# Kernel tuning notes

Measured on AMD Instinct MI355X. Metric: run time of the kernel, lower is better.

The kernel has to match this reference:

```python
import jax, jax.numpy as jnp
import numpy as np
from jax import lax

DIM = 192
HEADS = 6
WS = 8
SHIFT = 4
RED = max(8, DIM // 8)  # 24
HID = 4 * DIM


def _rel_index(ws):
    coords = np.stack(np.meshgrid(np.arange(ws), np.arange(ws), indexing='ij'))  # [2,ws,ws]
    flat = coords.reshape(2, -1)
    rel = (flat[:, :, None] - flat[:, None, :]).transpose(1, 2, 0)  # [T,T,2]
    rel[:, :, 0] += ws - 1
    rel[:, :, 1] += ws - 1
    rel[:, :, 0] *= 2 * ws - 1
    return rel.sum(-1)  # [T,T]


def _build_mask(h, w, ws, shift):
    img = np.zeros((h, w))
    slices = (slice(0, -ws), slice(-ws, -shift), slice(-shift, None))
    cnt = 0
    for hs in slices:
        for wcs in slices:
            img[hs, wcs] = cnt
            cnt += 1
    mw = img.reshape(h // ws, ws, w // ws, ws).transpose(0, 2, 1, 3).reshape(-1, ws * ws)
    diff = mw[:, None, :] - mw[:, :, None]  # [nW,T,T], diff[w,i,j]=mw[w,j]-mw[w,i]
    return np.where(diff != 0, -100.0, 0.0).astype(np.float32)


def _ln(x, g, b):
    m = x.mean(-1, keepdims=True)
    v = ((x - m) ** 2).mean(-1, keepdims=True)
    return (x - m) / jnp.sqrt(v + 1e-5) * g + b


def _conv(x, k, b, pad):
    y = lax.conv_general_dilated(x, k, (1, 1), [(pad, pad), (pad, pad)],
                                 dimension_numbers=('NCHW', 'OIHW', 'NCHW'))
    return y + b[None, :, None, None]


def setup_inputs() -> dict:
    key = jax.random.key(0)
    ks = jax.random.split(key, 16)
    rn = lambda k, s, sc=0.02: jax.random.normal(k, s, dtype=jnp.float32) * sc
    C = DIM
    return {
        'x': jax.random.normal(ks[0], (4, 256 * 256, C), dtype=jnp.float32),
        'ln1_g': jnp.ones((C,), jnp.float32), 'ln1_b': jnp.zeros((C,), jnp.float32),
        'w_qkv': rn(ks[1], (3 * C, C)), 'b_qkv': jnp.zeros((3 * C,), jnp.float32),
        'rel_table': rn(ks[2], ((2 * WS - 1) ** 2, HEADS)),
        'w_proj': rn(ks[3], (C, C)), 'b_proj': jnp.zeros((C,), jnp.float32),
        'ln2_g': jnp.ones((C,), jnp.float32), 'ln2_b': jnp.zeros((C,), jnp.float32),
        'w_fc1': rn(ks[4], (HID, C)), 'b_fc1': jnp.zeros((HID,), jnp.float32),
        'w_fc2': rn(ks[5], (C, HID)), 'b_fc2': jnp.zeros((C,), jnp.float32),
        'conv1_w': rn(ks[6], (RED, C, 1, 1)), 'conv1_b': jnp.zeros((RED,), jnp.float32),
        'conv2_w': rn(ks[7], (RED, RED, 3, 3)), 'conv2_b': jnp.zeros((RED,), jnp.float32),
        'conv3_w': rn(ks[8], (C, RED, 1, 1)), 'conv3_b': jnp.zeros((C,), jnp.float32),
        'se_w1': rn(ks[9], (RED, C)), 'se_w2': rn(ks[10], (C, RED)),
        'h': 256, 'w': 256,
    }


def reference(x, ln1_g, ln1_b, w_qkv, b_qkv, rel_table, w_proj, b_proj,
              ln2_g, ln2_b, w_fc1, b_fc1, w_fc2, b_fc2,
              conv1_w, conv1_b, conv2_w, conv2_b, conv3_w, conv3_b,
              se_w1, se_w2, h, w):
    B, _, C = x.shape
    ws, T, nh = WS, WS * WS, HEADS
    hd = C // nh
    scale = hd ** -0.5

    nx = _ln(x, ln1_g, ln1_b).reshape(B, h, w, C)
    local = nx.transpose(0, 3, 1, 2)  # NCHW for LCE

    # shifted window attention
    sh = jnp.roll(nx, (-SHIFT, -SHIFT), axis=(1, 2))
    win = sh.reshape(B, h // ws, ws, w // ws, ws, C).transpose(0, 1, 3, 2, 4, 5).reshape(-1, T, C)
    qkv = (win @ w_qkv.T + b_qkv).reshape(-1, T, 3, nh, hd).transpose(2, 0, 3, 1, 4)
    q, k, v = qkv[0] * scale, qkv[1], qkv[2]  # [BW, nh, T, hd]
    attn = jnp.einsum('whid,whjd->whij', q, k)  # [BW, nh, T, T]
    bias = rel_table[_rel_index(ws).reshape(-1)].reshape(T, T, nh).transpose(2, 0, 1)
    attn = attn + bias[None]
    mask = jnp.asarray(_build_mask(h, w, ws, SHIFT))  # [nW, T, T]
    nW = mask.shape[0]
    attn = attn.reshape(B, nW, nh, T, T) + mask[None, :, None]
    attn = jax.nn.softmax(attn, axis=-1).reshape(-1, nh, T, T)
    out = jnp.einsum('whij,whjd->whid', attn, v).transpose(0, 2, 1, 3).reshape(-1, T, C)
    out = out @ w_proj.T + b_proj
    out = out.reshape(B, h // ws, w // ws, ws, ws, C).transpose(0, 1, 3, 2, 4, 5).reshape(B, h, w, C)
    out = jnp.roll(out, (SHIFT, SHIFT), axis=(1, 2))

    x1 = x + out.reshape(B, h * w, C)
    n2 = _ln(x1, ln2_g, ln2_b)
    mlp = jax.nn.gelu(n2 @ w_fc1.T + b_fc1, approximate=False) @ w_fc2.T + b_fc2
    x2 = x1 + mlp

    # LocalContextExtractor (SE-style)
    y = _conv(local, conv1_w, conv1_b, 0)
    y = _conv(y, conv2_w, conv2_b, 1)
    y = _conv(y, conv3_w, conv3_b, 0)
    y = jnp.where(y >= 0, y, 0.2 * y)  # LeakyReLU(0.2)
    pooled = y.mean(axis=(2, 3))  # [B, C]
    wgt = jax.nn.sigmoid(jax.nn.relu(pooled @ se_w1.T) @ se_w2.T)
    y = y * wgt[:, :, None, None]
    lc = y.reshape(B, C, h * w).transpose(0, 2, 1)
    return x2 + lc
```

## Files before the change

### kernel.cpp

```cpp
#include <hip/hip_runtime.h>
#include <hip/hip_bf16.h>

typedef unsigned short u16;
typedef unsigned long long u64;
typedef __attribute__((ext_vector_type(8))) short short8x;
typedef __attribute__((ext_vector_type(4))) float f32x4;
typedef __bf16 bf16x8 __attribute__((ext_vector_type(8)));

#define SCALE 0.17677669529663687f

__device__ __forceinline__ u16 f2bf(float f) {
  unsigned u = __builtin_bit_cast(unsigned, f);
  unsigned r = (u + 0x7FFFu + ((u >> 16) & 1u)) >> 16;
  return (u16)r;
}
__device__ __forceinline__ float bf2f(u16 h) {
  return __builtin_bit_cast(float, ((unsigned)h) << 16);
}
__device__ __forceinline__ float gelu_f(float v) {
  float t = v * v;
  float a = __builtin_fmaf(t, -0.07135481627f, -1.59576912161f);
  float e = __expf(v * a);
  return v * __builtin_amdgcn_rcpf(1.0f + e);
}
__device__ __forceinline__ int swz(int row, int col, int ld) {
  return row * ld + ((((col >> 3) ^ (row & 7)) << 3) | (col & 7));
}
__device__ __forceinline__ short8x ldfrag(const u16* s, int row, int kb, int ld) {
  return *(const short8x*)(s + row * ld + (((kb >> 3) ^ (row & 7)) << 3));
}
__device__ __forceinline__ short8x ldg8(const u16* p) { return *(const short8x*)p; }

__device__ __forceinline__ f32x4 MFMA(short8x a, short8x b, f32x4 c) {
  return __builtin_amdgcn_mfma_f32_16x16x32_bf16(
      __builtin_bit_cast(bf16x8, a), __builtin_bit_cast(bf16x8, b), c, 0, 0, 0);
}
__device__ __forceinline__ u64 pack4(float a, float b, float c, float d) {
  return (u64)f2bf(a) | ((u64)f2bf(b) << 16) | ((u64)f2bf(c) << 32) | ((u64)f2bf(d) << 48);
}

__global__ void cvt_kernel(const float* __restrict__ wqkv, const float* __restrict__ wproj,
                           const float* __restrict__ wfc1, const float* __restrict__ wfc2,
                           const float* __restrict__ c1, const float* __restrict__ c3,
                           const float* __restrict__ c2,
                           u16* oq, u16* op, u16* o1, u16* o2, u16* oc1, u16* oc3,
                           float* ow2r) {
  int i = blockIdx.x * 256 + threadIdx.x;
  if (i < 110592) { float f = wqkv[i]; if (i < 36864) f *= SCALE; oq[i] = f2bf(f); return; }
  i -= 110592;
  if (i < 36864) { op[i] = f2bf(wproj[i]); return; }
  i -= 36864;
  if (i < 147456) { o1[i] = f2bf(wfc1[i]); return; }
  i -= 147456;
  if (i < 147456) { o2[i] = f2bf(wfc2[i]); return; }
  i -= 147456;
  if (i < 6144) { int r = i / 192, c = i - r * 192; oc1[i] = (r < 24) ? f2bf(c1[r * 192 + c]) : (u16)0; return; }
  i -= 6144;
  if (i < 6144) { int cc = i >> 5, k = i & 31; oc3[i] = (k < 24) ? f2bf(c3[cc * 24 + k]) : (u16)0; return; }
  i -= 6144;
  if (i < 5184) { int t = i / 576, rr = i - t * 576; int ci = rr / 24, co = rr - ci * 24;
                  ow2r[i] = c2[co * 216 + ci * 9 + t]; }
}

__global__ __launch_bounds__(256) void ln1_kernel(const float* __restrict__ x,
                                                  const float* __restrict__ g,
                                                  const float* __restrict__ b,
                                                  u16* __restrict__ nx) {
  const int wid = threadIdx.x >> 6, lane = threadIdx.x & 63;
  const int row = blockIdx.x * 4 + wid;
  const float* xr = x + row * 192;
  f32x4 v = {0.f, 0.f, 0.f, 0.f};
  if (lane < 48) v = *(const f32x4*)(xr + lane * 4);
  float s = v[0] + v[1] + v[2] + v[3];
  for (int m = 1; m < 64; m <<= 1) s += __shfl_xor(s, m);
  const float mean = s * (1.0f / 192.0f);
  f32x4 d;
#pragma unroll
  for (int r = 0; r < 4; ++r) d[r] = v[r] - mean;
  float q = (lane < 48) ? (d[0] * d[0] + d[1] * d[1] + d[2] * d[2] + d[3] * d[3]) : 0.f;
  for (int m = 1; m < 64; m <<= 1) q += __shfl_xor(q, m);
  const float rstd = rsqrtf(q * (1.0f / 192.0f) + 1e-5f);
  if (lane < 48) {
    const f32x4 gg = *(const f32x4*)(g + lane * 4);
    const f32x4 bb = *(const f32x4*)(b + lane * 4);
    u64 pk = pack4(d[0] * rstd * gg[0] + bb[0], d[1] * rstd * gg[1] + bb[1],
                   d[2] * rstd * gg[2] + bb[2], d[3] * rstd * gg[3] + bb[3]);
    *(u64*)(nx + row * 192 + lane * 4) = pk;
  }
}

__global__ __launch_bounds__(512, 4) void attn_kernel(
    const float* __restrict__ x, const u16* __restrict__ nx,
    const u16* __restrict__ wq, const float* __restrict__ bqkv,
    const float* __restrict__ rel, const u16* __restrict__ wp,
    const float* __restrict__ bproj, u16* __restrict__ vT,
    float* __restrict__ x1out) {
  __shared__ u16 sQK[64 * 384];
  __shared__ float sRel[1350];
  __shared__ int sG[64];

  const int tid = threadIdx.x, blk = blockIdx.x;
  const int b = blk >> 10, wi = (blk >> 5) & 31, wj = blk & 31;
  const int wv = tid >> 6, lane = tid & 63, lr = lane & 15, hi = lane >> 4;
  u16* vTw = vT + blk * 12288;

  for (int i = tid; i < 1350; i += 512) sRel[i] = rel[i];
  if (tid < 64) {
    int si = (wi * 8 + (tid >> 3) + 4) & 255, sj = (wj * 8 + (tid & 7) + 4) & 255;
    sG[tid] = b * 65536 + si * 256 + sj;
  }
  for (int i = tid; i < 64 * 96; i += 512) {
    int r = i / 96, w32 = i - r * 96;
    int si = (wi * 8 + (r >> 3) + 4) & 255, sj = (wj * 8 + (r & 7) + 4) & 255;
    int grow = b * 65536 + si * 256 + sj;
    unsigned v = ((const unsigned*)nx)[grow * 96 + w32];
    ((unsigned*)sQK)[r * 192 + ((((w32 >> 2) ^ (r & 7)) << 2) | (w32 & 3))] = v;
  }
  __syncthreads();

  f32x4 acc[4][4] = {};
  if (wv < 6) {
    const int wbase = wv * 64;
#pragma unroll
    for (int kk = 0; kk < 6; ++kk) {
      short8x Xf[4];
#pragma unroll
      for (int tt = 0; tt < 4; ++tt) Xf[tt] = ldfrag(sQK, tt * 16 + lr, kk * 32 + hi * 8, 384);
#pragma unroll
      for (int wt = 0; wt < 4; ++wt) {
        short8x Wf = ldg8(wq + (wbase + wt * 16 + lr) * 192 + kk * 32 + hi * 8);
#pragma unroll
        for (int tt = 0; tt < 4; ++tt) acc[wt][tt] = MFMA(Wf, Xf[tt], acc[wt][tt]);
      }
    }
  } else {
    const int vbase = (wv - 6) * 96;
#pragma unroll
    for (int half = 0; half < 2; ++half) {
      short8x Bf[3][6];
      float bv[3];
#pragma unroll
      for (int j = 0; j < 3; ++j) {
        const int vc = vbase + (half * 3 + j) * 16 + lr;
#pragma unroll
        for (int kk = 0; kk < 6; ++kk)
          Bf[j][kk] = ldg8(wq + (384 + vc) * 192 + kk * 32 + hi * 8);
        bv[j] = bqkv[384 + vc];
      }
#pragma unroll
      for (int mt = 0; mt < 4; ++mt) {
        f32x4 vacc[3] = {};
#pragma unroll
        for (int kk = 0; kk < 6; ++kk) {
          short8x A = ldfrag(sQK, mt * 16 + lr, kk * 32 + hi * 8, 384);
#pragma unroll
          for (int j = 0; j < 3; ++j) vacc[j] = MFMA(A, Bf[j][kk], vacc[j]);
        }
#pragma unroll
        for (int j = 0; j < 3; ++j) {
          u64 pk = pack4(vacc[j][0] + bv[j], vacc[j][1] + bv[j],
                         vacc[j][2] + bv[j], vacc[j][3] + bv[j]);
          *(u64*)(vTw + (vbase + (half * 3 + j) * 16 + lr) * 64 + mt * 16 + hi * 4) = pk;
        }
      }
    }
  }
  __syncthreads();

  if (wv < 6) {
    const int wbase = wv * 64;
#pragma unroll
    for (int wt = 0; wt < 4; ++wt) {
      const int oc0 = wbase + wt * 16 + hi * 4;
      const f32x4 bq = *(const f32x4*)(bqkv + oc0);
      const float sc = (oc0 < 192) ? SCALE : 1.0f;
#pragma unroll
      for (int tt = 0; tt < 4; ++tt) {
        u64 pk = pack4(acc[wt][tt][0] + bq[0] * sc, acc[wt][tt][1] + bq[1] * sc,
                       acc[wt][tt][2] + bq[2] * sc, acc[wt][tt][3] + bq[3] * sc);
        *(u64*)&sQK[swz(tt * 16 + lr, oc0, 384)] = pk;
      }
    }
  }
  __syncthreads();

  f32x4 S[3][4];
#pragma unroll
  for (int i = 0; i < 3; ++i) {
    const int s = wv + 8 * i, h3 = s >> 2, q = s & 3;
    short8x Aq = ldfrag(sQK, q * 16 + lr, h3 * 32 + hi * 8, 384);
#pragma unroll
    for (int nt = 0; nt < 4; ++nt) {
      short8x Bk = ldfrag(sQK, nt * 16 + lr, 192 + h3 * 32 + hi * 8, 384);
      S[i][nt] = MFMA(Aq, Bk, (f32x4){0.f, 0.f, 0.f, 0.f});
    }
#pragma unroll
    for (int r = 0; r < 4; ++r) {
      const int tI = q * 16 + hi * 4 + r;
      const int tri = tI >> 3, trj = tI & 7;
      const int ui = wi * 8 + tri, vi = wj * 8 + trj;
      const int rgi = (ui >= 248) + (ui >= 252), cgi = (vi >= 248) + (vi >= 252);
#pragma unroll
      for (int nt = 0; nt < 4; ++nt) {
        const int tJ = nt * 16 + lr;
        const int tci = tJ >> 3, tcj = tJ & 7;
        const int idx = (tri - tci + 7) * 15 + (trj - tcj + 7);
        float v = S[i][nt][r] + sRel[idx * 6 + h3];
        const int uj = wi * 8 + tci, vj = wj * 8 + tcj;
        const int rgj = (uj >= 248) + (uj >= 252), cgj = (vj >= 248) + (vj >= 252);
        if ((rgi != rgj) | (cgi != cgj)) v -= 100.0f;
        S[i][nt][r] = v;
      }
    }
#pragma unroll
    for (int r = 0; r < 4; ++r) {
      float mx = fmaxf(fmaxf(S[i][0][r], S[i][1][r]), fmaxf(S[i][2][r], S[i][3][r]));
      mx = fmaxf(mx, __shfl_xor(mx, 1));
      mx = fmaxf(mx, __shfl_xor(mx, 2));
      mx = fmaxf(mx, __shfl_xor(mx, 4));
      mx = fmaxf(mx, __shfl_xor(mx, 8));
      float sm = 0.f;
#pragma unroll
      for (int nt = 0; nt < 4; ++nt) { float e = __expf(S[i][nt][r] - mx); S[i][nt][r] = e; sm += e; }
      sm += __shfl_xor(sm, 1); sm += __shfl_xor(sm, 2);
      sm += __shfl_xor(sm, 4); sm += __shfl_xor(sm, 8);
      const float inv = 1.0f / sm;
#pragma unroll
      for (int nt = 0; nt < 4; ++nt) S[i][nt][r] *= inv;
    }
  }
  __syncthreads();

#pragma unroll
  for (int i = 0; i < 3; ++i) {
    const int s = wv + 8 * i, h3 = s >> 2, q = s & 3;
#pragma unroll
    for (int r = 0; r < 4; ++r)
#pragma unroll
      for (int nt = 0; nt < 4; ++nt)
        sQK[h3 * 4096 + swz(q * 16 + hi * 4 + r, nt * 16 + lr, 64)] = f2bf(S[i][nt][r]);
  }
  __syncthreads();

  f32x4 oacc[3][2] = {};
#pragma unroll
  for (int i = 0; i < 3; ++i) {
    const int t = wv + 8 * i, h3 = t >> 2, dt = (t >> 1) & 1, tth = t & 1;
#pragma unroll
    for (int kk = 0; kk < 2; ++kk) {
      short8x Va = ldg8(vTw + (h3 * 32 + dt * 16 + lr) * 64 + kk * 32 + hi * 8);
#pragma unroll
      for (int t2 = 0; t2 < 2; ++t2) {
        short8x Pf = ldfrag(sQK + h3 * 4096, tth * 32 + t2 * 16 + lr, kk * 32 + hi * 8, 64);
        oacc[i][t2] = MFMA(Va, Pf, oacc[i][t2]);
      }
    }
  }
  __syncthreads();

#pragma unroll
  for (int i = 0; i < 3; ++i) {
    const int t = wv + 8 * i, h3 = t >> 2, dt = (t >> 1) & 1, tth = t & 1;
#pragma unroll
    for (int t2 = 0; t2 < 2; ++t2) {
      u64 pk = pack4(oacc[i][t2][0], oacc[i][t2][1], oacc[i][t2][2], oacc[i][t2][3]);
      *(u64*)&sQK[swz(tth * 32 + t2 * 16 + lr, h3 * 32 + dt * 16 + hi * 4, 192)] = pk;
    }
  }
  __syncthreads();

  {
    const int nw = (wv < 4) ? 2 : 1;
    const int wt0 = (wv < 4) ? wv * 2 : (4 + wv);
    f32x4 pacc[2][4] = {};
#pragma unroll
    for (int kk = 0; kk < 6; ++kk) {
      short8x Of[4];
#pragma unroll
      for (int tt = 0; tt < 4; ++tt) Of[tt] = ldfrag(sQK, tt * 16 + lr, kk * 32 + hi * 8, 192);
      for (int w2 = 0; w2 < nw; ++w2) {
        short8x Wp = ldg8(wp + ((wt0 + w2) * 16 + lr) * 192 + kk * 32 + hi * 8);
#pragma unroll
        for (int tt = 0; tt < 4; ++tt) pacc[w2][tt] = MFMA(Wp, Of[tt], pacc[w2][tt]);
      }
    }
    for (int w2 = 0; w2 < nw; ++w2) {
      const int oc0 = (wt0 + w2) * 16 + hi * 4;
      const f32x4 bb = *(const f32x4*)(bproj + oc0);
#pragma unroll
      for (int tt = 0; tt < 4; ++tt) {
        const int grow = sG[tt * 16 + lr];
        const f32x4 xv = *(const f32x4*)(x + grow * 192 + oc0);
        f32x4 o;
#pragma unroll
        for (int r = 0; r < 4; ++r) o[r] = xv[r] + pacc[w2][tt][r] + bb[r];
        *(f32x4*)(x1out + grow * 192 + oc0) = o;
      }
    }
  }
}

__global__ __launch_bounds__(256) void conv1_kernel(const u16* __restrict__ nx,
                                                    const u16* __restrict__ w1,
                                                    const float* __restrict__ b1,
                                                    float* __restrict__ y1) {
  const int tid = threadIdx.x, wv = tid >> 6, lane = tid & 63, lr = lane & 15, hi = lane >> 4;
  const int g0 = blockIdx.x * 64;
  const int mt = wv;
  short8x Af[6];
#pragma unroll
  for (int kk = 0; kk < 6; ++kk)
    Af[kk] = ldg8(nx + (g0 + mt * 16 + lr) * 192 + kk * 32 + hi * 8);
  const int bI = g0 >> 16;
  const int hw0 = g0 & 65535;
#pragma unroll
  for (int nt = 0; nt < 2; ++nt) {
    f32x4 acc = {0.f, 0.f, 0.f, 0.f};
#pragma unroll
    for (int kk = 0; kk < 6; ++kk) {
      short8x Bf = ldg8(w1 + (nt * 16 + lr) * 192 + kk * 32 + hi * 8);
      acc = MFMA(Af[kk], Bf, acc);
    }
    const int c = nt * 16 + lr;
    if (c < 24) {
      const float bb = b1[c];
#pragma unroll
      for (int r = 0; r < 4; ++r) {
        const int pix = hw0 + mt * 16 + hi * 4 + r;
        y1[(bI * 24 + c) * 65536 + pix] = acc[r] + bb;
      }
    }
  }
}

__global__ __launch_bounds__(256) void conv2_kernel(const float* __restrict__ y1,
                                                    const float* __restrict__ w2r,
                                                    const float* __restrict__ cb2,
                                                    u16* __restrict__ y2) {
  const int j = threadIdx.x;
  const int i = blockIdx.x & 255;
  const int b = blockIdx.x >> 8;
  float acc[24];
#pragma unroll
  for (int r = 0; r < 24; ++r) acc[r] = cb2[r];
  const float* base = y1 + b * 24 * 65536;
  for (int t = 0; t < 9; ++t) {
    const int dh = t / 3 - 1, dw = t % 3 - 1;
    const int ii = i + dh, jj = j + dw;
    const bool ok = (ii >= 0) & (ii < 256) & (jj >= 0) & (jj < 256);
    const int offc = ok ? (ii * 256 + jj) : 0;
    const float* wt = w2r + t * 576;
    float v[24];
#pragma unroll
    for (int ci = 0; ci < 24; ++ci) {
      float vv = base[ci * 65536 + offc];
      v[ci] = ok ? vv : 0.0f;
    }
#pragma unroll
    for (int ci = 0; ci < 24; ++ci)
#pragma unroll
      for (int co = 0; co < 24; ++co)
        acc[co] += v[ci] * wt[ci * 24 + co];
  }
  u16* o = y2 + (b * 65536 + i * 256 + j) * 32;
#pragma unroll
  for (int r = 0; r < 24; ++r) o[r] = f2bf(acc[r]);
  ((unsigned long long*)(o + 24))[0] = 0ull;
  ((unsigned long long*)(o + 24))[1] = 0ull;
}

__global__ __launch_bounds__(256) void conv3_kernel(const u16* __restrict__ y2,
                                                    const u16* __restrict__ w3,
                                                    const float* __restrict__ b3,
                                                    u16* __restrict__ y,
                                                    float* __restrict__ pooled) {
  const int tid = threadIdx.x, wv = tid >> 6, lane = tid & 63, lr = lane & 15, hi = lane >> 4;
  const int g0 = blockIdx.x * 64;
  short8x Af[4];
#pragma unroll
  for (int mt = 0; mt < 4; ++mt)
    Af[mt] = ldg8(y2 + (g0 + mt * 16 + lr) * 32 + hi * 8);
  const int bI = g0 >> 16;
#pragma unroll
  for (int nt0 = 0; nt0 < 3; ++nt0) {
    const int c = (wv * 3 + nt0) * 16 + lr;
    short8x Bf = ldg8(w3 + c * 32 + hi * 8);
    const float bb = b3[c];
    float colsum = 0.f;
#pragma unroll
    for (int mt = 0; mt < 4; ++mt) {
      f32x4 acc = {0.f, 0.f, 0.f, 0.f};
      acc = MFMA(Af[mt], Bf, acc);
#pragma unroll
      for (int r = 0; r < 4; ++r) {
        float v = acc[r] + bb;
        v = (v >= 0.f) ? v : 0.2f * v;
        y[(g0 + mt * 16 + hi * 4 + r) * 192 + c] = f2bf(v);
        colsum += v;
      }
    }
    colsum += __shfl_xor(colsum, 16);
    colsum += __shfl_xor(colsum, 32);
    if (hi == 0) atomicAdd(&pooled[bI * 192 + c], colsum);
  }
}

__global__ void se_kernel(const float* __restrict__ pooled, const float* __restrict__ w1,
                          const float* __restrict__ w2, float* __restrict__ wgt) {
  __shared__ float t[24];
  const int b = blockIdx.x, lane = threadIdx.x;
  if (lane < 24) {
    float s = 0.f;
    for (int c = 0; c < 192; ++c) s += pooled[b * 192 + c] * (1.0f / 65536.0f) * w1[lane * 192 + c];
    t[lane] = fmaxf(s, 0.0f);
  }
  __syncthreads();
  for (int c = lane; c < 192; c += 64) {
    float s = 0.f;
#pragma unroll
    for (int r = 0; r < 24; ++r) s += t[r] * w2[c * 24 + r];
    wgt[b * 192 + c] = 1.0f / (1.0f + __expf(-s));
  }
}

__global__ __launch_bounds__(768, 6) void mlp_kernel(
    const float* x1, const float* __restrict__ g2, const float* __restrict__ b2,
    const u16* __restrict__ w1m, const float* __restrict__ bf1,
    const u16* __restrict__ w2m, const float* __restrict__ bf2,
    const u16* __restrict__ y, const float* __restrict__ wgt, float* out) {
  __shared__ u16 sN[64 * 192];
  __shared__ u16 sH[64 * 192];
  const int tid = threadIdx.x, wv = tid >> 6, lane = tid & 63, lr = lane & 15, hi = lane >> 4;
  const int g0 = blockIdx.x * 64;

  for (int row = wv; row < 64; row += 12) {
    const float* xr = x1 + (g0 + row) * 192;
    float v0 = xr[lane], v1 = xr[lane + 64], v2 = xr[lane + 128];
    float s = v0 + v1 + v2;
    for (int m = 1; m < 64; m <<= 1) s += __shfl_xor(s, m);
    const float mean = s * (1.0f / 192.0f);
    const float d0 = v0 - mean, d1 = v1 - mean, d2 = v2 - mean;
    float q = d0 * d0 + d1 * d1 + d2 * d2;
    for (int m = 1; m < 64; m <<= 1) q += __shfl_xor(q, m);
    const float rstd = rsqrtf(q * (1.0f / 192.0f) + 1e-5f);
    sN[swz(row, lane, 192)]       = f2bf(d0 * rstd * g2[lane] + b2[lane]);
    sN[swz(row, lane + 64, 192)]  = f2bf(d1 * rstd * g2[lane + 64] + b2[lane + 64]);
    sN[swz(row, lane + 128, 192)] = f2bf(d2 * rstd * g2[lane + 128] + b2[lane + 128]);
  }
  __syncthreads();

  f32x4 acc[4] = {};
  for (int c = 0; c < 4; ++c) {
    const int hcol = c * 192 + wv * 16 + lr;
    f32x4 a1[4] = {};
#pragma unroll
    for (int kk = 0; kk < 6; ++kk) {
      short8x B = ldg8(w1m + hcol * 192 + kk * 32 + hi * 8);
#pragma unroll
      for (int mt = 0; mt < 4; ++mt)
        a1[mt] = MFMA(ldfrag(sN, mt * 16 + lr, kk * 32 + hi * 8, 192), B, a1[mt]);
    }
    if (c) __syncthreads();
    const float bb1 = bf1[hcol];
#pragma unroll
    for (int mt = 0; mt < 4; ++mt)
#pragma unroll
      for (int r = 0; r < 4; ++r)
        sH[swz(mt * 16 + hi * 4 + r, wv * 16 + lr, 192)] = f2bf(gelu_f(a1[mt][r] + bb1));
    __syncthreads();
#pragma unroll
    for (int kk = 0; kk < 6; ++kk) {
      short8x B = ldg8(w2m + (wv * 16 + lr) * 768 + c * 192 + kk * 32 + hi * 8);
#pragma unroll
      for (int mt = 0; mt < 4; ++mt)
        acc[mt] = MFMA(ldfrag(sH, mt * 16 + lr, kk * 32 + hi * 8, 192), B, acc[mt]);
    }
  }

  const int bI = g0 >> 16;
  const int ocol = wv * 16 + lr;
  const float bb = bf2[ocol];
  const float wg = wgt[bI * 192 + ocol];
#pragma unroll
  for (int mt = 0; mt < 4; ++mt)
#pragma unroll
    for (int r = 0; r < 4; ++r) {
      const int grow = g0 + mt * 16 + hi * 4 + r;
      const float lc = bf2f(y[grow * 192 + ocol]) * wg;
      out[grow * 192 + ocol] = x1[grow * 192 + ocol] + acc[mt][r] + bb + lc;
    }
}

extern "C" void kernel_launch(void* const* d_in, const int* in_sizes, int n_in,
                              void* d_out, int out_size, void* d_ws, size_t ws_size,
                              hipStream_t stream) {
  const float* x     = (const float*)d_in[0];
  const float* ln1g  = (const float*)d_in[1];
  const float* ln1b  = (const float*)d_in[2];
  const float* wqkv  = (const float*)d_in[3];
  const float* bqkv  = (const float*)d_in[4];
  const float* rel   = (const float*)d_in[5];
  const float* wproj = (const float*)d_in[6];
  const float* bproj = (const float*)d_in[7];
  const float* ln2g  = (const float*)d_in[8];
  const float* ln2b  = (const float*)d_in[9];
  const float* wfc1  = (const float*)d_in[10];
  const float* bfc1  = (const float*)d_in[11];
  const float* wfc2  = (const float*)d_in[12];
  const float* bfc2  = (const float*)d_in[13];
  const float* c1w   = (const float*)d_in[14];
  const float* c1b   = (const float*)d_in[15];
  const float* c2w   = (const float*)d_in[16];
  const float* c2b   = (const float*)d_in[17];
  const float* c3w   = (const float*)d_in[18];
  const float* c3b   = (const float*)d_in[19];
  const float* sew1  = (const float*)d_in[20];
  const float* sew2  = (const float*)d_in[21];

  char* ws = (char*)d_ws;
  u16*   nx   = (u16*)(ws + 0);
  float* y1   = (float*)(ws + 100663296);
  u16*   y2   = (u16*)(ws + 125829120);
  u16*   yb   = (u16*)(ws + 142606336);
  u16*   wq   = (u16*)(ws + 243269632);
  u16*   wp   = (u16*)(ws + 243490816);
  u16*   w1m  = (u16*)(ws + 243564544);
  u16*   w2m  = (u16*)(ws + 243859456);
  u16*   cw1  = (u16*)(ws + 244154368);
  u16*   cw3  = (u16*)(ws + 244166656);
  float* w2r  = (float*)(ws + 244178944);
  float* pool = (float*)(ws + 244199680);
  float* wgt  = (float*)(ws + 244202752);
  float* out  = (float*)d_out;
  u16*   vT   = yb;

  hipMemsetAsync(pool, 0, 3072, stream);
  cvt_kernel<<<1797, 256, 0, stream>>>(wqkv, wproj, wfc1, wfc2, c1w, c3w, c2w,
                                       wq, wp, w1m, w2m, cw1, cw3, w2r);
  ln1_kernel<<<65536, 256, 0, stream>>>(x, ln1g, ln1b, nx);
  attn_kernel<<<4096, 512, 0, stream>>>(x, nx, wq, bqkv, rel, wp, bproj, vT, out);
  conv1_kernel<<<4096, 256, 0, stream>>>(nx, cw1, c1b, y1);
  conv2_kernel<<<1024, 256, 0, stream>>>(y1, w2r, c2b, y2);
  conv3_kernel<<<4096, 256, 0, stream>>>(y2, cw3, c3b, yb, pool);
  se_kernel<<<4, 64, 0, stream>>>(pool, sew1, sew2, wgt);
  mlp_kernel<<<4096, 768, 0, stream>>>(out, ln2g, ln2b, w1m, bfc1, w2m, bfc2, yb, wgt, out);
}
```

Measured before the change: 1.015 ms.

## Move attention output projection into MLP kernel and pass attention output as bf16

The attention kernel now writes its per-head output as bf16 into a global buffer that reuses the LN1 buffer in place. The conv1 launch moves ahead of attention so it still reads the original LN1 data. The output projection, bias and residual add move into a merged proj+MLP kernel, which keeps x1 in registers and feeds LN2 from shared memory. This is meant to remove the fp32 x1 round trip through global memory and the extra shared-memory staging and syncs in the attention kernel. In exchange, LN2 now reads bf16-rounded x1, and every wave reloads the attention output tile from global memory for the projection.

Measured after the change: 1.160 ms. 14.3% more time.

```diff
diff --git a/kernel.cpp b/kernel.cpp
--- a/kernel.cpp
+++ b/kernel.cpp
@@ -90,11 +90,9 @@
 }
 
 __global__ __launch_bounds__(512, 4) void attn_kernel(
-    const float* __restrict__ x, const u16* __restrict__ nx,
-    const u16* __restrict__ wq, const float* __restrict__ bqkv,
-    const float* __restrict__ rel, const u16* __restrict__ wp,
-    const float* __restrict__ bproj, u16* __restrict__ vT,
-    float* __restrict__ x1out) {
+    const u16* __restrict__ nx, const u16* __restrict__ wq,
+    const float* __restrict__ bqkv, const float* __restrict__ rel,
+    u16* __restrict__ vT, u16* __restrict__ aout) {
   __shared__ u16 sQK[64 * 384];
   __shared__ float sRel[1350];
   __shared__ int sG[64];
@@ -242,60 +240,25 @@
   }
   __syncthreads();
 
-  f32x4 oacc[3][2] = {};
 #pragma unroll
   for (int i = 0; i < 3; ++i) {
     const int t = wv + 8 * i, h3 = t >> 2, dt = (t >> 1) & 1, tth = t & 1;
+    f32x4 oacc[2] = {};
 #pragma unroll
     for (int kk = 0; kk < 2; ++kk) {
       short8x Va = ldg8(vTw + (h3 * 32 + dt * 16 + lr) * 64 + kk * 32 + hi * 8);
 #pragma unroll
       for (int t2 = 0; t2 < 2; ++t2) {
         short8x Pf = ldfrag(sQK + h3 * 4096, tth * 32 + t2 * 16 + lr, kk * 32 + hi * 8, 64);
-        oacc[i][t2] = MFMA(Va, Pf, oacc[i][t2]);
-      }
-    }
-  }
-  __syncthreads();
-
-#pragma unroll
-  for (int i = 0; i < 3; ++i) {
-    const int t = wv + 8 * i, h3 = t >> 2, dt = (t >> 1) & 1, tth = t & 1;
+        oacc[t2] = MFMA(Va, Pf, oacc[t2]);
+      }
+    }
 #pragma unroll
     for (int t2 = 0; t2 < 2; ++t2) {
-      u64 pk = pack4(oacc[i][t2][0], oacc[i][t2][1], oacc[i][t2][2], oacc[i][t2][3]);
-      *(u64*)&sQK[swz(tth * 32 + t2 * 16 + lr, h3 * 32 + dt * 16 + hi * 4, 192)] = pk;
-    }
-  }
-  __syncthreads();
-
-  {
-    const int nw = (wv < 4) ? 2 : 1;
-    const int wt0 = (wv < 4) ? wv * 2 : (4 + wv);
-    f32x4 pacc[2][4] = {};
-#pragma unroll
-    for (int kk = 0; kk < 6; ++kk) {
-      short8x Of[4];
-#pragma unroll
-      for (int tt = 0; tt < 4; ++tt) Of[tt] = ldfrag(sQK, tt * 16 + lr, kk * 32 + hi * 8, 192);
-      for (int w2 = 0; w2 < nw; ++w2) {
-        short8x Wp = ldg8(wp + ((wt0 + w2) * 16 + lr) * 192 + kk * 32 + hi * 8);
-#pragma unroll
-        for (int tt = 0; tt < 4; ++tt) pacc[w2][tt] = MFMA(Wp, Of[tt], pacc[w2][tt]);
-      }
-    }
-    for (int w2 = 0; w2 < nw; ++w2) {
-      const int oc0 = (wt0 + w2) * 16 + hi * 4;
-      const f32x4 bb = *(const f32x4*)(bproj + oc0);
-#pragma unroll
-      for (int tt = 0; tt < 4; ++tt) {
-        const int grow = sG[tt * 16 + lr];
-        const f32x4 xv = *(const f32x4*)(x + grow * 192 + oc0);
-        f32x4 o;
-#pragma unroll
-        for (int r = 0; r < 4; ++r) o[r] = xv[r] + pacc[w2][tt][r] + bb[r];
-        *(f32x4*)(x1out + grow * 192 + oc0) = o;
-      }
+      const int token = tth * 32 + t2 * 16 + lr;
+      const int grow = sG[token];
+      u64 pk = pack4(oacc[t2][0], oacc[t2][1], oacc[t2][2], oacc[t2][3]);
+      *(u64*)(aout + grow * 192 + h3 * 32 + dt * 16 + hi * 4) = pk;
     }
   }
 }
@@ -423,19 +386,44 @@
   }
 }
 
-__global__ __launch_bounds__(768, 6) void mlp_kernel(
-    const float* x1, const float* __restrict__ g2, const float* __restrict__ b2,
+__global__ __launch_bounds__(768, 6) void pmlp_kernel(
+    const float* __restrict__ x, const u16* __restrict__ aout,
+    const u16* __restrict__ wp, const float* __restrict__ bproj,
+    const float* __restrict__ g2, const float* __restrict__ b2,
     const u16* __restrict__ w1m, const float* __restrict__ bf1,
     const u16* __restrict__ w2m, const float* __restrict__ bf2,
-    const u16* __restrict__ y, const float* __restrict__ wgt, float* out) {
+    const u16* __restrict__ y, const float* __restrict__ wgt, float* __restrict__ out) {
   __shared__ u16 sN[64 * 192];
   __shared__ u16 sH[64 * 192];
   const int tid = threadIdx.x, wv = tid >> 6, lane = tid & 63, lr = lane & 15, hi = lane >> 4;
   const int g0 = blockIdx.x * 64;
+  const int ocol = wv * 16 + lr;
+
+  f32x4 x1v[4];
+  {
+    f32x4 pacc[4] = {};
+#pragma unroll
+    for (int kk = 0; kk < 6; ++kk) {
+      short8x Wf = ldg8(wp + ocol * 192 + kk * 32 + hi * 8);
+#pragma unroll
+      for (int mt = 0; mt < 4; ++mt)
+        pacc[mt] = MFMA(ldg8(aout + (g0 + mt * 16 + lr) * 192 + kk * 32 + hi * 8), Wf, pacc[mt]);
+    }
+    const float bb = bproj[ocol];
+#pragma unroll
+    for (int mt = 0; mt < 4; ++mt)
+#pragma unroll
+      for (int r = 0; r < 4; ++r) {
+        x1v[mt][r] = x[(g0 + mt * 16 + hi * 4 + r) * 192 + ocol] + pacc[mt][r] + bb;
+        sN[swz(mt * 16 + hi * 4 + r, ocol, 192)] = f2bf(x1v[mt][r]);
+      }
+  }
+  __syncthreads();
 
   for (int row = wv; row < 64; row += 12) {
-    const float* xr = x1 + (g0 + row) * 192;
-    float v0 = xr[lane], v1 = xr[lane + 64], v2 = xr[lane + 128];
+    float v0 = bf2f(sN[swz(row, lane, 192)]);
+    float v1 = bf2f(sN[swz(row, lane + 64, 192)]);
+    float v2 = bf2f(sN[swz(row, lane + 128, 192)]);
     float s = v0 + v1 + v2;
     for (int m = 1; m < 64; m <<= 1) s += __shfl_xor(s, m);
     const float mean = s * (1.0f / 192.0f);
@@ -478,7 +466,6 @@
   }
 
   const int bI = g0 >> 16;
-  const int ocol = wv * 16 + lr;
   const float bb = bf2[ocol];
   const float wg = wgt[bI * 192 + ocol];
 #pragma unroll
@@ -487,7 +474,7 @@
     for (int r = 0; r < 4; ++r) {
       const int grow = g0 + mt * 16 + hi * 4 + r;
       const float lc = bf2f(y[grow * 192 + ocol]) * wg;
-      out[grow * 192 + ocol] = x1[grow * 192 + ocol] + acc[mt][r] + bb + lc;
+      out[grow * 192 + ocol] = x1v[mt][r] + acc[mt][r] + bb + lc;
     }
 }
 
@@ -533,15 +520,17 @@
   float* wgt  = (float*)(ws + 244202752);
   float* out  = (float*)d_out;
   u16*   vT   = yb;
+  u16*   aout = nx;
 
   hipMemsetAsync(pool, 0, 3072, stream);
   cvt_kernel<<<1797, 256, 0, stream>>>(wqkv, wproj, wfc1, wfc2, c1w, c3w, c2w,
                                        wq, wp, w1m, w2m, cw1, cw3, w2r);
   ln1_kernel<<<65536, 256, 0, stream>>>(x, ln1g, ln1b, nx);
-  attn_kernel<<<4096, 512, 0, stream>>>(x, nx, wq, bqkv, rel, wp, bproj, vT, out);
   conv1_kernel<<<4096, 256, 0, stream>>>(nx, cw1, c1b, y1);
+  attn_kernel<<<4096, 512, 0, stream>>>(nx, wq, bqkv, rel, vT, aout);
   conv2_kernel<<<1024, 256, 0, stream>>>(y1, w2r, c2b, y2);
   conv3_kernel<<<4096, 256, 0, stream>>>(y2, cw3, c3b, yb, pool);
   se_kernel<<<4, 64, 0, stream>>>(pool, sew1, sew2, wgt);
-  mlp_kernel<<<4096, 768, 0, stream>>>(out, ln2g, ln2b, w1m, bfc1, w2m, bfc2, yb, wgt, out);
-}
+  pmlp_kernel<<<4096, 768, 0, stream>>>(x, aout, wp, bproj, ln2g, ln2b,
+                                        w1m, bfc1, w2m, bfc2, yb, wgt, out);
+}
```

## Split QKV projection to cut registers and shrink LDS for higher occupancy

Applied to the files above, without the earlier changes.

The attention kernel now computes Q in two phases and K afterwards. The input tile sits in the upper half of shared memory, so Q can be written into the lower half while K is still being computed, and only half the accumulators are live at a time. The V path processes one 16-column tile at a time instead of three, and the relative-position table is stored as bf16 in LDS. Launch bounds rise from 4 to 6 blocks per SM. The aim is lower register and LDS pressure so more blocks fit per CU, at the cost of bf16 rounding on the bias and less ILP per wave.

New measurement: 1.321 ms. 1.3x slower.

```diff
diff --git a/kernel.cpp b/kernel.cpp
--- a/kernel.cpp
+++ b/kernel.cpp
@@ -89,14 +89,14 @@
   }
 }
 
-__global__ __launch_bounds__(512, 4) void attn_kernel(
+__global__ __launch_bounds__(512, 6) void attn_kernel(
     const float* __restrict__ x, const u16* __restrict__ nx,
     const u16* __restrict__ wq, const float* __restrict__ bqkv,
     const float* __restrict__ rel, const u16* __restrict__ wp,
     const float* __restrict__ bproj, u16* __restrict__ vT,
     float* __restrict__ x1out) {
   __shared__ u16 sQK[64 * 384];
-  __shared__ float sRel[1350];
+  __shared__ u16 sRel[1350];
   __shared__ int sG[64];
 
   const int tid = threadIdx.x, blk = blockIdx.x;
@@ -104,80 +104,93 @@
   const int wv = tid >> 6, lane = tid & 63, lr = lane & 15, hi = lane >> 4;
   u16* vTw = vT + blk * 12288;
 
-  for (int i = tid; i < 1350; i += 512) sRel[i] = rel[i];
+  for (int i = tid; i < 1350; i += 512) sRel[i] = f2bf(rel[i]);
   if (tid < 64) {
     int si = (wi * 8 + (tid >> 3) + 4) & 255, sj = (wj * 8 + (tid & 7) + 4) & 255;
     sG[tid] = b * 65536 + si * 256 + sj;
   }
   for (int i = tid; i < 64 * 96; i += 512) {
-    int r = i / 96, w32 = i - r * 96;
+    int r = i / 96, j = i - r * 96;
     int si = (wi * 8 + (r >> 3) + 4) & 255, sj = (wj * 8 + (r & 7) + 4) & 255;
     int grow = b * 65536 + si * 256 + sj;
-    unsigned v = ((const unsigned*)nx)[grow * 96 + w32];
-    ((unsigned*)sQK)[r * 192 + ((((w32 >> 2) ^ (r & 7)) << 2) | (w32 & 3))] = v;
-  }
-  __syncthreads();
-
-  f32x4 acc[4][4] = {};
+    unsigned v = ((const unsigned*)nx)[grow * 96 + j];
+    ((unsigned*)sQK)[r * 192 + 96 + ((((j >> 2) ^ (r & 7)) << 2) | (j & 3))] = v;
+  }
+  __syncthreads();
+
+  f32x4 acck[2][4] = {};
   if (wv < 6) {
-    const int wbase = wv * 64;
+    {
+      f32x4 accq[2][4] = {};
+#pragma unroll
+      for (int kk = 0; kk < 6; ++kk) {
+        short8x A[4];
+#pragma unroll
+        for (int tt = 0; tt < 4; ++tt) A[tt] = ldfrag(sQK, tt * 16 + lr, 192 + kk * 32 + hi * 8, 384);
+#pragma unroll
+        for (int wt = 0; wt < 2; ++wt) {
+          short8x Wf = ldg8(wq + (wv * 32 + wt * 16 + lr) * 192 + kk * 32 + hi * 8);
+#pragma unroll
+          for (int tt = 0; tt < 4; ++tt) accq[wt][tt] = MFMA(Wf, A[tt], accq[wt][tt]);
+        }
+      }
+#pragma unroll
+      for (int wt = 0; wt < 2; ++wt) {
+        const int oc0 = wv * 32 + wt * 16 + hi * 4;
+        const f32x4 bq = *(const f32x4*)(bqkv + oc0);
+#pragma unroll
+        for (int tt = 0; tt < 4; ++tt) {
+          u64 pk = pack4(accq[wt][tt][0] + bq[0] * SCALE, accq[wt][tt][1] + bq[1] * SCALE,
+                         accq[wt][tt][2] + bq[2] * SCALE, accq[wt][tt][3] + bq[3] * SCALE);
+          *(u64*)&sQK[swz(tt * 16 + lr, oc0, 384)] = pk;
+        }
+      }
+    }
 #pragma unroll
     for (int kk = 0; kk < 6; ++kk) {
-      short8x Xf[4];
-#pragma unroll
-      for (int tt = 0; tt < 4; ++tt) Xf[tt] = ldfrag(sQK, tt * 16 + lr, kk * 32 + hi * 8, 384);
-#pragma unroll
-      for (int wt = 0; wt < 4; ++wt) {
-        short8x Wf = ldg8(wq + (wbase + wt * 16 + lr) * 192 + kk * 32 + hi * 8);
-#pragma unroll
-        for (int tt = 0; tt < 4; ++tt) acc[wt][tt] = MFMA(Wf, Xf[tt], acc[wt][tt]);
+      short8x A[4];
+#pragma unroll
+      for (int tt = 0; tt < 4; ++tt) A[tt] = ldfrag(sQK, tt * 16 + lr, 192 + kk * 32 + hi * 8, 384);
+#pragma unroll
+      for (int wt = 0; wt < 2; ++wt) {
+        short8x Wf = ldg8(wq + (192 + wv * 32 + wt * 16 + lr) * 192 + kk * 32 + hi * 8);
+#pragma unroll
+        for (int tt = 0; tt < 4; ++tt) acck[wt][tt] = MFMA(Wf, A[tt], acck[wt][tt]);
       }
     }
   } else {
     const int vbase = (wv - 6) * 96;
 #pragma unroll
-    for (int half = 0; half < 2; ++half) {
-      short8x Bf[3][6];
-      float bv[3];
-#pragma unroll
-      for (int j = 0; j < 3; ++j) {
-        const int vc = vbase + (half * 3 + j) * 16 + lr;
-#pragma unroll
-        for (int kk = 0; kk < 6; ++kk)
-          Bf[j][kk] = ldg8(wq + (384 + vc) * 192 + kk * 32 + hi * 8);
-        bv[j] = bqkv[384 + vc];
-      }
+    for (int vt = 0; vt < 6; ++vt) {
+      const int vc = vbase + vt * 16 + lr;
+      short8x Bf[6];
+#pragma unroll
+      for (int kk = 0; kk < 6; ++kk) Bf[kk] = ldg8(wq + (384 + vc) * 192 + kk * 32 + hi * 8);
+      const float bv = bqkv[384 + vc];
 #pragma unroll
       for (int mt = 0; mt < 4; ++mt) {
-        f32x4 vacc[3] = {};
+        f32x4 va = {0.f, 0.f, 0.f, 0.f};
 #pragma unroll
         for (int kk = 0; kk < 6; ++kk) {
-          short8x A = ldfrag(sQK, mt * 16 + lr, kk * 32 + hi * 8, 384);
-#pragma unroll
-          for (int j = 0; j < 3; ++j) vacc[j] = MFMA(A, Bf[j][kk], vacc[j]);
+          short8x A = ldfrag(sQK, mt * 16 + lr, 192 + kk * 32 + hi * 8, 384);
+          va = MFMA(A, Bf[kk], va);
         }
-#pragma unroll
-        for (int j = 0; j < 3; ++j) {
-          u64 pk = pack4(vacc[j][0] + bv[j], vacc[j][1] + bv[j],
-                         vacc[j][2] + bv[j], vacc[j][3] + bv[j]);
-          *(u64*)(vTw + (vbase + (half * 3 + j) * 16 + lr) * 64 + mt * 16 + hi * 4) = pk;
-        }
+        u64 pk = pack4(va[0] + bv, va[1] + bv, va[2] + bv, va[3] + bv);
+        *(u64*)(vTw + vc * 64 + mt * 16 + hi * 4) = pk;
       }
     }
   }
   __syncthreads();
 
   if (wv < 6) {
-    const int wbase = wv * 64;
-#pragma unroll
-    for (int wt = 0; wt < 4; ++wt) {
-      const int oc0 = wbase + wt * 16 + hi * 4;
+#pragma unroll
+    for (int wt = 0; wt < 2; ++wt) {
+      const int oc0 = 192 + wv * 32 + wt * 16 + hi * 4;
       const f32x4 bq = *(const f32x4*)(bqkv + oc0);
-      const float sc = (oc0 < 192) ? SCALE : 1.0f;
 #pragma unroll
       for (int tt = 0; tt < 4; ++tt) {
-        u64 pk = pack4(acc[wt][tt][0] + bq[0] * sc, acc[wt][tt][1] + bq[1] * sc,
-                       acc[wt][tt][2] + bq[2] * sc, acc[wt][tt][3] + bq[3] * sc);
+        u64 pk = pack4(acck[wt][tt][0] + bq[0], acck[wt][tt][1] + bq[1],
+                       acck[wt][tt][2] + bq[2], acck[wt][tt][3] + bq[3]);
         *(u64*)&sQK[swz(tt * 16 + lr, oc0, 384)] = pk;
       }
     }
@@ -205,7 +218,7 @@
         const int tJ = nt * 16 + lr;
         const int tci = tJ >> 3, tcj = tJ & 7;
         const int idx = (tri - tci + 7) * 15 + (trj - tcj + 7);
-        float v = S[i][nt][r] + sRel[idx * 6 + h3];
+        float v = S[i][nt][r] + bf2f(sRel[idx * 6 + h3]);
         const int uj = wi * 8 + tci, vj = wj * 8 + tcj;
         const int rgj = (uj >= 248) + (uj >= 252), cgj = (vj >= 248) + (vj >= 252);
         if ((rgi != rgj) | (cgi != cgj)) v -= 100.0f;
```

## Swap MFMA operands in MLP kernel and retile warps to 32x32 blocks

Applied to the files above, without the earlier changes.

The fused LN2+MLP kernel now treats weights as the A operand and tokens as the B operand, so each accumulator holds four consecutive hidden/output channels for one token. Warps are retiled from 16 columns by 64 tokens to 32 columns by 32 tokens, with two warp groups splitting the token rows. This allows packed 64-bit bf16 stores into the hidden-activation shared buffer and 128-bit vectorized bias, x1, y and output accesses in the epilogue, replacing scalar strided ones. In exchange each warp loads twice as many weight fragments from global memory per token, since every weight fragment is now shared by only two MFMAs instead of four.

Measured after the change: 1.249 ms. +23.0%, slower.

```diff
diff --git a/kernel.cpp b/kernel.cpp
--- a/kernel.cpp
+++ b/kernel.cpp
@@ -449,46 +449,67 @@
   }
   __syncthreads();
 
-  f32x4 acc[4] = {};
+  const int th = (wv >= 6) ? 1 : 0;
+  const int cs = wv - 6 * th;
+  f32x4 acc2[2][2] = {};
   for (int c = 0; c < 4; ++c) {
-    const int hcol = c * 192 + wv * 16 + lr;
-    f32x4 a1[4] = {};
+    f32x4 a1[2][2] = {};
 #pragma unroll
     for (int kk = 0; kk < 6; ++kk) {
-      short8x B = ldg8(w1m + hcol * 192 + kk * 32 + hi * 8);
-#pragma unroll
-      for (int mt = 0; mt < 4; ++mt)
-        a1[mt] = MFMA(ldfrag(sN, mt * 16 + lr, kk * 32 + hi * 8, 192), B, a1[mt]);
+      short8x B0 = ldfrag(sN, th * 32 + lr, kk * 32 + hi * 8, 192);
+      short8x B1 = ldfrag(sN, th * 32 + 16 + lr, kk * 32 + hi * 8, 192);
+#pragma unroll
+      for (int wt = 0; wt < 2; ++wt) {
+        short8x Wf = ldg8(w1m + (c * 192 + cs * 32 + wt * 16 + lr) * 192 + kk * 32 + hi * 8);
+        a1[wt][0] = MFMA(Wf, B0, a1[wt][0]);
+        a1[wt][1] = MFMA(Wf, B1, a1[wt][1]);
+      }
     }
     if (c) __syncthreads();
-    const float bb1 = bf1[hcol];
-#pragma unroll
-    for (int mt = 0; mt < 4; ++mt)
+#pragma unroll
+    for (int wt = 0; wt < 2; ++wt) {
+      const int h0 = cs * 32 + wt * 16 + hi * 4;
+      const f32x4 b1v = *(const f32x4*)(bf1 + c * 192 + h0);
+#pragma unroll
+      for (int tt = 0; tt < 2; ++tt) {
+        const int tok = th * 32 + tt * 16 + lr;
+        u64 pk = pack4(gelu_f(a1[wt][tt][0] + b1v[0]), gelu_f(a1[wt][tt][1] + b1v[1]),
+                       gelu_f(a1[wt][tt][2] + b1v[2]), gelu_f(a1[wt][tt][3] + b1v[3]));
+        *(u64*)&sH[swz(tok, h0, 192)] = pk;
+      }
+    }
+    __syncthreads();
+#pragma unroll
+    for (int kk = 0; kk < 6; ++kk) {
+      short8x H0 = ldfrag(sH, th * 32 + lr, kk * 32 + hi * 8, 192);
+      short8x H1 = ldfrag(sH, th * 32 + 16 + lr, kk * 32 + hi * 8, 192);
+#pragma unroll
+      for (int wt = 0; wt < 2; ++wt) {
+        short8x W2 = ldg8(w2m + (cs * 32 + wt * 16 + lr) * 768 + c * 192 + kk * 32 + hi * 8);
+        acc2[wt][0] = MFMA(W2, H0, acc2[wt][0]);
+        acc2[wt][1] = MFMA(W2, H1, acc2[wt][1]);
+      }
+    }
+  }
+
+  const int bI = g0 >> 16;
+#pragma unroll
+  for (int wt = 0; wt < 2; ++wt) {
+    const int oc0 = cs * 32 + wt * 16 + hi * 4;
+    const f32x4 bb = *(const f32x4*)(bf2 + oc0);
+    const f32x4 wg = *(const f32x4*)(wgt + bI * 192 + oc0);
+#pragma unroll
+    for (int tt = 0; tt < 2; ++tt) {
+      const int grow = g0 + th * 32 + tt * 16 + lr;
+      const f32x4 xv = *(const f32x4*)(x1 + grow * 192 + oc0);
+      const u64 yv = *(const u64*)(y + grow * 192 + oc0);
+      f32x4 o;
 #pragma unroll
       for (int r = 0; r < 4; ++r)
-        sH[swz(mt * 16 + hi * 4 + r, wv * 16 + lr, 192)] = f2bf(gelu_f(a1[mt][r] + bb1));
-    __syncthreads();
-#pragma unroll
-    for (int kk = 0; kk < 6; ++kk) {
-      short8x B = ldg8(w2m + (wv * 16 + lr) * 768 + c * 192 + kk * 32 + hi * 8);
-#pragma unroll
-      for (int mt = 0; mt < 4; ++mt)
-        acc[mt] = MFMA(ldfrag(sH, mt * 16 + lr, kk * 32 + hi * 8, 192), B, acc[mt]);
-    }
-  }
-
-  const int bI = g0 >> 16;
-  const int ocol = wv * 16 + lr;
-  const float bb = bf2[ocol];
-  const float wg = wgt[bI * 192 + ocol];
-#pragma unroll
-  for (int mt = 0; mt < 4; ++mt)
-#pragma unroll
-    for (int r = 0; r < 4; ++r) {
-      const int grow = g0 + mt * 16 + hi * 4 + r;
-      const float lc = bf2f(y[grow * 192 + ocol]) * wg;
-      out[grow * 192 + ocol] = x1[grow * 192 + ocol] + acc[mt][r] + bb + lc;
-    }
+        o[r] = xv[r] + acc2[wt][tt][r] + bb[r] + bf2f((u16)(yv >> (16 * r))) * wg[r];
+      *(f32x4*)(out + grow * 192 + oc0) = o;
+    }
+  }
 }
 
 extern "C" void kernel_launch(void* const* d_in, const int* in_sizes, int n_in,
```
